# Kernel tuning notes

Measured on AMD Instinct MI355X. Metric: run time of the kernel, lower is better.

Reference implementation:

```python
import jax, jax.numpy as jnp
import numpy as np

N_EMBD = 2048
N_HEAD = 16
HEAD_DIM = N_EMBD // N_HEAD
BATCH = 2
SEQ = 2048


def setup_inputs() -> dict:
    key = jax.random.key(0)
    k1, k2, k3 = jax.random.split(key, 3)
    scale = 0.02
    return {
        "hidden_states": jax.random.normal(k1, (BATCH, SEQ, N_EMBD), dtype=jnp.float32),
        "c_attn_w": jax.random.normal(k2, (N_EMBD, 3 * N_EMBD), dtype=jnp.float32) * scale,
        "c_attn_b": jnp.zeros((3 * N_EMBD,), dtype=jnp.float32),
        "c_proj_w": jax.random.normal(k3, (N_EMBD, N_EMBD), dtype=jnp.float32) * scale,
        "c_proj_b": jnp.zeros((N_EMBD,), dtype=jnp.float32),
    }


def reference(hidden_states, c_attn_w, c_attn_b, c_proj_w, c_proj_b):
    B, S, E = hidden_states.shape
    # Fused QKV projection (Conv1D: x @ W + b)
    qkv = hidden_states @ c_attn_w + c_attn_b  # [B, S, 3E]
    q, k, v = jnp.split(qkv, 3, axis=-1)
    # split heads -> [B, H, S, D]
    def split_heads(t):
        return t.reshape(B, S, N_HEAD, HEAD_DIM).transpose(0, 2, 1, 3)
    q, k, v = split_heads(q), split_heads(k), split_heads(v)
    # scaled scores, causal mask, softmax (dropout p=0 -> identity)
    scores = jnp.einsum("bhqd,bhkd->bhqk", q, k) / jnp.asarray(
        HEAD_DIM ** 0.5, dtype=q.dtype)
    causal = jnp.tril(jnp.ones((S, S), dtype=bool))  # [S, S]
    mask_value = jnp.finfo(scores.dtype).min
    scores = jnp.where(causal[None, None, :, :], scores, mask_value)
    attn = jax.nn.softmax(scores, axis=-1)
    out = jnp.einsum("bhqk,bhkd->bhqd", attn, v)  # [B, H, S, D]
    # merge heads -> [B, S, E]
    out = out.transpose(0, 2, 1, 3).reshape(B, S, E)
    # output projection
    return out @ c_proj_w + c_proj_b
```

## Files before the change

kernel.cpp:

```cpp
#include <hip/hip_runtime.h>
#include <hip/hip_bf16.h>

typedef __bf16 bf16x8 __attribute__((ext_vector_type(8)));
typedef float f32x4 __attribute__((ext_vector_type(4)));

__device__ __forceinline__ float bf2f(unsigned short u) {
  union { unsigned int i; float f; } v; v.i = ((unsigned int)u) << 16; return v.f;
}
__device__ __forceinline__ unsigned short f2bf(float f) {
  union { unsigned int i; float f; } v; v.f = f;
  unsigned int i = v.i;
  return (unsigned short)((i + 0x7FFFu + ((i >> 16) & 1u)) >> 16);
}

typedef const __attribute__((address_space(1))) unsigned int* gas_ptr;
typedef __attribute__((address_space(3))) unsigned int* las_ptr;
__device__ __forceinline__ void gload_lds16(const unsigned short* g, unsigned short* l) {
  __builtin_amdgcn_global_load_lds((gas_ptr)(const void*)g, (las_ptr)(void*)l, 16, 0, 0);
}

__global__ __launch_bounds__(256) void detect_k(const unsigned short* __restrict__ h,
                                                int* __restrict__ flag) {
  __shared__ int s[256];
  int cnt = 0;
  for (int i = threadIdx.x; i < 4096; i += 256) {
    unsigned short u = h[2 * i];
    int e = (u >> 7) & 0xFF;
    if ((e >= 96 && e <= 140) || u == 0) cnt++;
  }
  s[threadIdx.x] = cnt;
  __syncthreads();
  for (int o = 128; o > 0; o >>= 1) {
    if (threadIdx.x < o) s[threadIdx.x] += s[threadIdx.x + o];
    __syncthreads();
  }
  if (threadIdx.x == 0) *flag = (s[0] >= 3600) ? 1 : 0;
}

__global__ __launch_bounds__(256) void cvt_hidden_k(const void* __restrict__ src,
                                                    unsigned short* __restrict__ dst, int n,
                                                    const int* __restrict__ flag) {
  if (*flag) return;
  for (int i = blockIdx.x * 256 + threadIdx.x; i < n; i += gridDim.x * 256)
    dst[i] = f2bf(((const float*)src)[i]);
}

__global__ __launch_bounds__(256) void transpose_w2_k(const void* __restrict__ w_qkv,
                                                      const void* __restrict__ w_proj,
                                                      unsigned short* __restrict__ dst_qkv,
                                                      unsigned short* __restrict__ dst_proj,
                                                      const int* __restrict__ flag) {
  __shared__ unsigned short tile[32][33];
  const int f = *flag;
  int bid = blockIdx.x;
  const void* src;
  unsigned short* dst;
  int R = 2048, C, cx, cy;
  if (bid < 12288) {
    src = w_qkv; dst = dst_qkv; C = 6144; cx = bid % 192; cy = bid / 192;
  } else {
    bid -= 12288;
    src = w_proj; dst = dst_proj; C = 2048; cx = bid % 64; cy = bid / 64;
  }
  const int x = threadIdx.x & 31;
  const int y = threadIdx.x >> 5;
  const int r0 = cy * 32, c0 = cx * 32;
#pragma unroll
  for (int i = 0; i < 4; i++) {
    size_t idx = (size_t)(r0 + y + 8 * i) * C + c0 + x;
    tile[y + 8 * i][x] = f ? ((const unsigned short*)src)[idx]
                           : f2bf(((const float*)src)[idx]);
  }
  __syncthreads();
#pragma unroll
  for (int i = 0; i < 4; i++)
    dst[(size_t)(c0 + y + 8 * i) * R + r0 + x] = tile[x][y + 8 * i];
}

__global__ __launch_bounds__(256) void transpose_v_k(const unsigned short* __restrict__ qkv,
                                                     unsigned short* __restrict__ Vt) {
  __shared__ unsigned short tile[32][33];
  const int bh = blockIdx.z;
  const int b = bh >> 4, hh = bh & 15;
  const int s0 = blockIdx.x * 32, d0 = blockIdx.y * 32;
  const int x = threadIdx.x & 31, y = threadIdx.x >> 5;
#pragma unroll
  for (int i = 0; i < 4; i++)
    tile[y + 8 * i][x] =
        qkv[((size_t)b * 2048 + s0 + y + 8 * i) * 6144 + 4096 + hh * 128 + d0 + x];
  __syncthreads();
#pragma unroll
  for (int i = 0; i < 4; i++)
    Vt[((size_t)bh * 128 + d0 + y + 8 * i) * 2048 + s0 + x] = tile[x][y + 8 * i];
}

__global__ __launch_bounds__(256) void gemm_bias_k(const unsigned short* __restrict__ A_bf,
                                                   const unsigned short* __restrict__ A_cvt,
                                                   const unsigned short* __restrict__ Bt,
                                                   const void* __restrict__ bias,
                                                   void* __restrict__ Cout,
                                                   int M, int N, int K,
                                                   const int* __restrict__ flag,
                                                   int final_out) {
  __shared__ __attribute__((aligned(16))) unsigned short As[128][64];
  __shared__ __attribute__((aligned(16))) unsigned short Bs[128][64];
  const int f = *flag;
  const unsigned short* A = f ? A_bf : A_cvt;
  const int t = threadIdx.x;
  const int wave = t >> 6, lane = t & 63;
  const int col = lane & 15, quad = lane >> 4;
  const int wm = wave >> 1, wn = wave & 1;
  const int m0 = blockIdx.y * 128, n0 = blockIdx.x * 128;
  const int srow = lane >> 3;
  const int schunk = ((lane & 7) ^ srow) * 8;
  const int rsw = col & 7;

  const f32x4 fzero = {0.f, 0.f, 0.f, 0.f};
  f32x4 acc[4][4];
#pragma unroll
  for (int i = 0; i < 4; i++)
#pragma unroll
    for (int j = 0; j < 4; j++) acc[i][j] = fzero;

  for (int k0 = 0; k0 < K; k0 += 64) {
    __syncthreads();
#pragma unroll
    for (int c = 0; c < 4; c++) {
      int seg = wave * 4 + c;
      int row = seg * 8 + srow;
      gload_lds16(&A [(size_t)(m0 + row) * K + k0 + schunk], &As[seg * 8][0]);
      gload_lds16(&Bt[(size_t)(n0 + row) * K + k0 + schunk], &Bs[seg * 8][0]);
    }
    __syncthreads();
#pragma unroll
    for (int ks = 0; ks < 2; ks++) {
      bf16x8 af[4], bfr[4];
#pragma unroll
      for (int i = 0; i < 4; i++)
        af[i] = *(const bf16x8*)&As[wm * 64 + i * 16 + col][(((ks << 2) | quad) ^ rsw) * 8];
#pragma unroll
      for (int j = 0; j < 4; j++)
        bfr[j] = *(const bf16x8*)&Bs[wn * 64 + j * 16 + col][(((ks << 2) | quad) ^ rsw) * 8];
#pragma unroll
      for (int i = 0; i < 4; i++)
#pragma unroll
        for (int j = 0; j < 4; j++)
          acc[i][j] = __builtin_amdgcn_mfma_f32_16x16x32_bf16(af[i], bfr[j], acc[i][j], 0, 0, 0);
    }
  }
  const int f32o = final_out ? (f == 0) : 0;
#pragma unroll
  for (int j = 0; j < 4; j++) {
    int n = n0 + wn * 64 + j * 16 + col;
    float bv = f ? bf2f(((const unsigned short*)bias)[n]) : ((const float*)bias)[n];
#pragma unroll
    for (int i = 0; i < 4; i++)
#pragma unroll
      for (int r = 0; r < 4; r++) {
        int m = m0 + wm * 64 + i * 16 + quad * 4 + r;
        float v = acc[i][j][r] + bv;
        if (f32o) ((float*)Cout)[(size_t)m * N + n] = v;
        else      ((unsigned short*)Cout)[(size_t)m * N + n] = f2bf(v);
      }
  }
}

#define ATT_SCALE 0.08838834764831845f
__global__ __launch_bounds__(256) void attn_k(const unsigned short* __restrict__ qkv,
                                              const unsigned short* __restrict__ Vt,
                                              unsigned short* __restrict__ O) {
  __shared__ __attribute__((aligned(16))) unsigned short Ks[64][136];
  __shared__ __attribute__((aligned(16))) unsigned short Vs[128][72];
  __shared__ __attribute__((aligned(16))) unsigned short Ps[4][16][72];
  const int t = threadIdx.x;
  const int wave = t >> 6, lane = t & 63;
  const int col = lane & 15, quad = lane >> 4;
  const int h = blockIdx.y, b = blockIdx.z;
  const size_t base = (size_t)b * 2048 * 6144;
  const size_t vbase = ((size_t)(b * 16 + h)) * 128 * 2048;
  const int hcol = h * 128;

  const int kr = t >> 2;
  const int kc = (t & 3) * 8;
  const int vr = t >> 1;
  const int vc = (t & 1) * 32;

  const f32x4 fzero = {0.f, 0.f, 0.f, 0.f};

  for (int pass = 0; pass < 2; pass++) {
    const int qt = pass ? (int)blockIdx.x : 31 - (int)blockIdx.x;

    bf16x8 qf[4];
    {
      size_t qrow = base + (size_t)(qt * 64 + wave * 16 + col) * 6144 + hcol;
#pragma unroll
      for (int ks = 0; ks < 4; ks++)
        qf[ks] = *(const bf16x8*)&qkv[qrow + ks * 32 + quad * 8];
    }

    f32x4 o[8];
#pragma unroll
    for (int i = 0; i < 8; i++) o[i] = fzero;
    float l_i[4] = {0.f, 0.f, 0.f, 0.f};

    __syncthreads();
    {
      size_t grow = base + (size_t)kr * 6144 + 2048 + hcol;
#pragma unroll
      for (int p = 0; p < 4; p++)
        *(bf16x8*)&Ks[kr][kc + p * 32] = *(const bf16x8*)&qkv[grow + kc + p * 32];
      size_t vrow = vbase + (size_t)vr * 2048;
#pragma unroll
      for (int c = 0; c < 4; c++)
        *(bf16x8*)&Vs[vr][vc + c * 8] = *(const bf16x8*)&Vt[vrow + vc + c * 8];
    }
    __syncthreads();

    for (int kt = 0; kt <= qt; kt++) {
      bf16x8 kreg[4], vreg[4];
      const bool pf = (kt < qt);
      if (pf) {
        size_t grow = base + (size_t)((kt + 1) * 64 + kr) * 6144 + 2048 + hcol;
#pragma unroll
        for (int p = 0; p < 4; p++)
          kreg[p] = *(const bf16x8*)&qkv[grow + kc + p * 32];
        size_t vrow = vbase + (size_t)vr * 2048 + (kt + 1) * 64;
#pragma unroll
        for (int c = 0; c < 4; c++)
          vreg[c] = *(const bf16x8*)&Vt[vrow + vc + c * 8];
      }

      f32x4 sc[4];
#pragma unroll
      for (int nb = 0; nb < 4; nb++) {
        f32x4 s = fzero;
#pragma unroll
        for (int ks = 0; ks < 4; ks++) {
          bf16x8 kf = *(const bf16x8*)&Ks[nb * 16 + col][ks * 32 + quad * 8];
          s = __builtin_amdgcn_mfma_f32_16x16x32_bf16(qf[ks], kf, s, 0, 0, 0);
        }
        sc[nb] = s;
      }

      const bool diag = (kt == qt);
#pragma unroll
      for (int nb = 0; nb < 4; nb++) {
        int kl = nb * 16 + col;
#pragma unroll
        for (int r = 0; r < 4; r++) {
          float s = sc[nb][r];
          if (diag && kl > wave * 16 + quad * 4 + r) s = -1e30f;
          float p = __expf(s * ATT_SCALE);
          l_i[r] += p;
          Ps[wave][quad * 4 + r][nb * 16 + col] = f2bf(p);
        }
      }
      bf16x8 pfr[2];
#pragma unroll
      for (int ks2 = 0; ks2 < 2; ks2++)
        pfr[ks2] = *(const bf16x8*)&Ps[wave][col][ks2 * 32 + quad * 8];
#pragma unroll
      for (int nbo = 0; nbo < 8; nbo++)
#pragma unroll
        for (int ks2 = 0; ks2 < 2; ks2++) {
          bf16x8 vf = *(const bf16x8*)&Vs[nbo * 16 + col][ks2 * 32 + quad * 8];
          o[nbo] = __builtin_amdgcn_mfma_f32_16x16x32_bf16(pfr[ks2], vf, o[nbo], 0, 0, 0);
        }

      __syncthreads();
      if (pf) {
#pragma unroll
        for (int p = 0; p < 4; p++)
          *(bf16x8*)&Ks[kr][kc + p * 32] = kreg[p];
#pragma unroll
        for (int c = 0; c < 4; c++)
          *(bf16x8*)&Vs[vr][vc + c * 8] = vreg[c];
      }
      __syncthreads();
    }

#pragma unroll
    for (int r = 0; r < 4; r++) {
#pragma unroll
      for (int off = 1; off < 16; off <<= 1)
        l_i[r] += __shfl_xor(l_i[r], off, 64);
      l_i[r] = 1.0f / l_i[r];
    }

#pragma unroll
    for (int nbo = 0; nbo < 8; nbo++)
#pragma unroll
      for (int r = 0; r < 4; r++) {
        int m = qt * 64 + wave * 16 + quad * 4 + r;
        O[((size_t)b * 2048 + m) * 2048 + hcol + nbo * 16 + col] = f2bf(o[nbo][r] * l_i[r]);
      }
  }
}

extern "C" void kernel_launch(void* const* d_in, const int* in_sizes, int n_in,
                              void* d_out, int out_size, void* d_ws, size_t ws_size,
                              hipStream_t stream) {
  (void)in_sizes; (void)n_in; (void)out_size; (void)ws_size;
  int* flag = (int*)d_ws;
  unsigned short* wsu = (unsigned short*)d_ws + 128;
  unsigned short* Wt_qkv    = wsu;
  unsigned short* Wt_proj   = Wt_qkv + (size_t)6144 * 2048;
  unsigned short* QKV       = Wt_proj + (size_t)2048 * 2048;
  unsigned short* hidden_bf = QKV + (size_t)4096 * 6144;
  unsigned short* Obuf      = Wt_qkv;
  unsigned short* Vt        = hidden_bf + (size_t)4096 * 2048;

  detect_k<<<1, 256, 0, stream>>>((const unsigned short*)d_in[0], flag);
  cvt_hidden_k<<<2048, 256, 0, stream>>>(d_in[0], hidden_bf, 4096 * 2048, flag);
  transpose_w2_k<<<16384, 256, 0, stream>>>(d_in[1], d_in[3], Wt_qkv, Wt_proj, flag);
  gemm_bias_k<<<dim3(48, 32), 256, 0, stream>>>((const unsigned short*)d_in[0], hidden_bf,
                                                Wt_qkv, d_in[2], QKV,
                                                4096, 6144, 2048, flag, 0);
  transpose_v_k<<<dim3(64, 4, 32), 256, 0, stream>>>(QKV, Vt);
  attn_k<<<dim3(16, 16, 2), 256, 0, stream>>>(QKV, Vt, Obuf);
  gemm_bias_k<<<dim3(16, 32), 256, 0, stream>>>(Obuf, Obuf, Wt_proj, d_in[4], d_out,
                                                4096, 2048, 2048, flag, 1);
}
```

Baseline: 415.9 us.

## Add 256x256-tile double-buffered MFMA GEMM kernel for the QKV projection

Adds a new GEMM kernel with 256x256 output tiles computed by 512 threads (8 waves). It double-buffers LDS via direct global-to-LDS loads, uses an XOR-swizzled shared layout, and remaps workgroup IDs into 8 chunks for better L2 locality. Loads for the next k-tile are interleaved with MFMA phases, and s_setprio raises priority during the MFMA phases. The QKV projection uses this kernel in place of the 128x128 version, aiming for higher arithmetic intensity and better latency hiding. The cost is more LDS (128KB) and more accumulator registers, which limits occupancy, and the grid is 384 blocks.

Result: no change. 423.6 us (+1.9%).

```diff
diff --git a/kernel.cpp b/kernel.cpp
--- a/kernel.cpp
+++ b/kernel.cpp
@@ -92,6 +92,163 @@
 #pragma unroll
   for (int i = 0; i < 4; i++)
     Vt[((size_t)bh * 128 + d0 + y + 8 * i) * 2048 + s0 + x] = tile[x][y + 8 * i];
+}
+
+__global__ __launch_bounds__(512, 2) void gemm256_k(const unsigned short* __restrict__ A_bf,
+                                                    const unsigned short* __restrict__ A_cvt,
+                                                    const unsigned short* __restrict__ Bt,
+                                                    const void* __restrict__ bias,
+                                                    unsigned short* __restrict__ Cout,
+                                                    int M, int N, int K,
+                                                    const int* __restrict__ flag) {
+  __shared__ __attribute__((aligned(16))) unsigned short As[2][2][128][64];
+  __shared__ __attribute__((aligned(16))) unsigned short Bs[2][2][128][64];
+  const int f = *flag;
+  const unsigned short* Ap = f ? A_bf : A_cvt;
+  const int t = threadIdx.x;
+  const int wave = t >> 6, lane = t & 63;
+  const int col = lane & 15, quad = lane >> 4;
+  const int wm = wave >> 2, wn = wave & 3;
+
+  const int nbx = N >> 8;
+  int wgid = blockIdx.y * nbx + blockIdx.x;
+  const int nwg = (M >> 8) * nbx;
+  if ((nwg & 7) == 0) {
+    const int cpx = nwg >> 3;
+    wgid = (wgid & 7) * cpx + (wgid >> 3);
+  }
+  const int n0 = (wgid % nbx) << 8;
+  const int m0 = (wgid / nbx) << 8;
+
+  const int srow = lane >> 3;
+  const int sx = ((lane & 7) ^ srow) * 8;
+  const int rsw = col & 7;
+
+  const unsigned short* pA = Ap + (size_t)(m0 + wave * 16 + srow) * K + sx;
+  const unsigned short* pB = Bt + (size_t)(n0 + wave * 16 + srow) * K + sx;
+  const int NT = K >> 6;
+
+#define STAGE_A(d, h, kt)                                                                  \
+  do {                                                                                     \
+    gload_lds16(pA + (size_t)((h) * 128) * K + (kt) * 64, &As[(d)][(h)][wave * 16][0]);    \
+    gload_lds16(pA + (size_t)((h) * 128 + 8) * K + (kt) * 64,                              \
+                &As[(d)][(h)][wave * 16 + 8][0]);                                          \
+  } while (0)
+#define STAGE_B(d, h, kt)                                                                  \
+  do {                                                                                     \
+    gload_lds16(pB + (size_t)((h) * 128) * K + (kt) * 64, &Bs[(d)][(h)][wave * 16][0]);    \
+    gload_lds16(pB + (size_t)((h) * 128 + 8) * K + (kt) * 64,                              \
+                &Bs[(d)][(h)][wave * 16 + 8][0]);                                          \
+  } while (0)
+#define LDA(d, rf, kk) \
+  (*(const bf16x8*)&As[(d)][wm][(rf) * 16 + col][((((kk) << 2) | quad) ^ rsw) * 8])
+#define LDB(d, cf, kk) \
+  (*(const bf16x8*)&Bs[(d)][wn >> 1][(wn & 1) * 64 + (cf) * 16 + col][((((kk) << 2) | quad) ^ rsw) * 8])
+
+  const f32x4 fzero = {0.f, 0.f, 0.f, 0.f};
+  f32x4 acc[8][4];
+#pragma unroll
+  for (int i = 0; i < 8; i++)
+#pragma unroll
+    for (int j = 0; j < 4; j++) acc[i][j] = fzero;
+
+  STAGE_A(0, 0, 0); STAGE_A(0, 1, 0);
+  STAGE_B(0, 0, 0); STAGE_B(0, 1, 0);
+  STAGE_A(1, 0, 1); STAGE_A(1, 1, 1);
+  asm volatile("s_waitcnt vmcnt(4)" ::: "memory");
+  __builtin_amdgcn_sched_barrier(0);
+  __builtin_amdgcn_s_barrier();
+
+  for (int u = 0; u < NT; ++u) {
+    const int d = u & 1;
+    bf16x8 a0[4][2], a1[4][2], b0[2][2], b1[2][2];
+
+#pragma unroll
+    for (int rf = 0; rf < 4; rf++) { a0[rf][0] = LDA(d, rf, 0); a0[rf][1] = LDA(d, rf, 1); }
+#pragma unroll
+    for (int cf = 0; cf < 2; cf++) { b0[cf][0] = LDB(d, cf, 0); b0[cf][1] = LDB(d, cf, 1); }
+    if (u + 1 < NT) STAGE_B(d ^ 1, 0, u + 1);
+    __builtin_amdgcn_s_barrier();
+    asm volatile("s_waitcnt lgkmcnt(0)" ::: "memory");
+    __builtin_amdgcn_sched_barrier(0);
+    __builtin_amdgcn_s_setprio(1);
+#pragma unroll
+    for (int rf = 0; rf < 4; rf++)
+#pragma unroll
+      for (int cf = 0; cf < 2; cf++) {
+        acc[rf][cf] = __builtin_amdgcn_mfma_f32_16x16x32_bf16(a0[rf][0], b0[cf][0], acc[rf][cf], 0, 0, 0);
+        acc[rf][cf] = __builtin_amdgcn_mfma_f32_16x16x32_bf16(a0[rf][1], b0[cf][1], acc[rf][cf], 0, 0, 0);
+      }
+    __builtin_amdgcn_s_setprio(0);
+    __builtin_amdgcn_s_barrier();
+
+#pragma unroll
+    for (int rf = 0; rf < 4; rf++) { a1[rf][0] = LDA(d, rf + 4, 0); a1[rf][1] = LDA(d, rf + 4, 1); }
+    if (u + 1 < NT) STAGE_B(d ^ 1, 1, u + 1);
+    __builtin_amdgcn_s_barrier();
+    asm volatile("s_waitcnt lgkmcnt(0)" ::: "memory");
+    __builtin_amdgcn_sched_barrier(0);
+    __builtin_amdgcn_s_setprio(1);
+#pragma unroll
+    for (int rf = 0; rf < 4; rf++)
+#pragma unroll
+      for (int cf = 0; cf < 2; cf++) {
+        acc[rf + 4][cf] = __builtin_amdgcn_mfma_f32_16x16x32_bf16(a1[rf][0], b0[cf][0], acc[rf + 4][cf], 0, 0, 0);
+        acc[rf + 4][cf] = __builtin_amdgcn_mfma_f32_16x16x32_bf16(a1[rf][1], b0[cf][1], acc[rf + 4][cf], 0, 0, 0);
+      }
+    __builtin_amdgcn_s_setprio(0);
+    __builtin_amdgcn_s_barrier();
+
+#pragma unroll
+    for (int cf = 0; cf < 2; cf++) { b1[cf][0] = LDB(d, cf + 2, 0); b1[cf][1] = LDB(d, cf + 2, 1); }
+    if (u + 2 < NT) STAGE_A(d, 0, u + 2);
+    __builtin_amdgcn_s_barrier();
+    asm volatile("s_waitcnt lgkmcnt(0)" ::: "memory");
+    __builtin_amdgcn_sched_barrier(0);
+    __builtin_amdgcn_s_setprio(1);
+#pragma unroll
+    for (int rf = 0; rf < 4; rf++)
+#pragma unroll
+      for (int cf = 0; cf < 2; cf++) {
+        acc[rf][cf + 2] = __builtin_amdgcn_mfma_f32_16x16x32_bf16(a0[rf][0], b1[cf][0], acc[rf][cf + 2], 0, 0, 0);
+        acc[rf][cf + 2] = __builtin_amdgcn_mfma_f32_16x16x32_bf16(a0[rf][1], b1[cf][1], acc[rf][cf + 2], 0, 0, 0);
+      }
+    __builtin_amdgcn_s_setprio(0);
+    __builtin_amdgcn_s_barrier();
+
+    if (u + 2 < NT) STAGE_A(d, 1, u + 2);
+    __builtin_amdgcn_s_setprio(1);
+#pragma unroll
+    for (int rf = 0; rf < 4; rf++)
+#pragma unroll
+      for (int cf = 0; cf < 2; cf++) {
+        acc[rf + 4][cf + 2] = __builtin_amdgcn_mfma_f32_16x16x32_bf16(a1[rf][0], b1[cf][0], acc[rf + 4][cf + 2], 0, 0, 0);
+        acc[rf + 4][cf + 2] = __builtin_amdgcn_mfma_f32_16x16x32_bf16(a1[rf][1], b1[cf][1], acc[rf + 4][cf + 2], 0, 0, 0);
+      }
+    __builtin_amdgcn_s_setprio(0);
+    if (u + 2 < NT) asm volatile("s_waitcnt vmcnt(4)" ::: "memory");
+    else            asm volatile("s_waitcnt vmcnt(0)" ::: "memory");
+    __builtin_amdgcn_sched_barrier(0);
+    __builtin_amdgcn_s_barrier();
+  }
+#undef STAGE_A
+#undef STAGE_B
+#undef LDA
+#undef LDB
+
+  const int nbase = n0 + wn * 64;
+#pragma unroll
+  for (int cf = 0; cf < 4; cf++) {
+    int n = nbase + cf * 16 + col;
+    float bv = f ? bf2f(((const unsigned short*)bias)[n]) : ((const float*)bias)[n];
+#pragma unroll
+    for (int rf = 0; rf < 8; rf++)
+#pragma unroll
+      for (int r = 0; r < 4; r++) {
+        int m = m0 + wm * 128 + rf * 16 + quad * 4 + r;
+        Cout[(size_t)m * N + n] = f2bf(acc[rf][cf][r] + bv);
+      }
+  }
 }
 
 __global__ __launch_bounds__(256) void gemm_bias_k(const unsigned short* __restrict__ A_bf,
@@ -313,9 +470,9 @@
   detect_k<<<1, 256, 0, stream>>>((const unsigned short*)d_in[0], flag);
   cvt_hidden_k<<<2048, 256, 0, stream>>>(d_in[0], hidden_bf, 4096 * 2048, flag);
   transpose_w2_k<<<16384, 256, 0, stream>>>(d_in[1], d_in[3], Wt_qkv, Wt_proj, flag);
-  gemm_bias_k<<<dim3(48, 32), 256, 0, stream>>>((const unsigned short*)d_in[0], hidden_bf,
-                                                Wt_qkv, d_in[2], QKV,
-                                                4096, 6144, 2048, flag, 0);
+  gemm256_k<<<dim3(24, 16), 512, 0, stream>>>((const unsigned short*)d_in[0], hidden_bf,
+                                              Wt_qkv, d_in[2], QKV,
+                                              4096, 6144, 2048, flag);
   transpose_v_k<<<dim3(64, 4, 32), 256, 0, stream>>>(QKV, Vt);
   attn_k<<<dim3(16, 16, 2), 256, 0, stream>>>(QKV, Vt, Obuf);
   gemm_bias_k<<<dim3(16, 32), 256, 0, stream>>>(Obuf, Obuf, Wt_proj, d_in[4], d_out,
```

## Add dedicated QKV GEMM kernel with 256x192 tiles and double-buffered async LDS pipeline

Applied to the files above, without the earlier changes.

Replaces the generic 128x128 GEMM for the QKV projection with a dedicated 512-thread kernel using 256x192 tiles. It double-buffers A and B in LDS through direct global-to-LDS loads with XOR swizzling, and interleaves staging with MFMA phases under explicit waitcnt, barriers and setprio. It also remaps workgroup IDs in an XCD-aware way to improve L2 locality. The aim is to hide memory latency and raise MFMA utilisation, at the cost of complex hand-tuned vmcnt/lgkmcnt counts that must stay exactly right, plus higher LDS and register use.

After: 389.1 us. 6.4% less time.

```diff
diff --git a/kernel.cpp b/kernel.cpp
--- a/kernel.cpp
+++ b/kernel.cpp
@@ -92,6 +92,166 @@
 #pragma unroll
   for (int i = 0; i < 4; i++)
     Vt[((size_t)bh * 128 + d0 + y + 8 * i) * 2048 + s0 + x] = tile[x][y + 8 * i];
+}
+
+__global__ __launch_bounds__(512, 2) void gemm_qkv_k(const unsigned short* __restrict__ A_bf,
+                                                     const unsigned short* __restrict__ A_cvt,
+                                                     const unsigned short* __restrict__ Bt,
+                                                     const void* __restrict__ bias,
+                                                     unsigned short* __restrict__ Cout,
+                                                     int M, int N, int K,
+                                                     const int* __restrict__ flag) {
+  __shared__ __attribute__((aligned(16))) unsigned short As[2][256][64];
+  __shared__ __attribute__((aligned(16))) unsigned short Bs[2][192][64];
+  const int f = *flag;
+  const unsigned short* Ap = f ? A_bf : A_cvt;
+  const int t = threadIdx.x;
+  const int wave = t >> 6, lane = t & 63;
+  const int col = lane & 15, quad = lane >> 4;
+  const int wm = wave >> 1, wn = wave & 1;
+
+  const int nbx = N / 192;
+  int wgid = blockIdx.y * nbx + blockIdx.x;
+  const int nwg = (M >> 8) * nbx;
+  if ((nwg & 7) == 0) {
+    const int cpx = nwg >> 3;
+    wgid = (wgid & 7) * cpx + (wgid >> 3);
+  }
+  const int n0 = (wgid % nbx) * 192;
+  const int m0 = (wgid / nbx) << 8;
+
+  const int srow = lane >> 3;
+  const int sx = ((lane & 7) ^ srow) * 8;
+  const int rsw = col & 7;
+
+  const unsigned short* pA = Ap + (size_t)(m0 + wave * 8 + srow) * K + sx;
+  const unsigned short* pB = Bt + (size_t)(n0 + wave * 8 + srow) * K + sx;
+  const int NT = K >> 6;
+
+#define STAGE_A(d, q, kt) \
+  gload_lds16(pA + (size_t)((q) * 64) * K + (size_t)(kt) * 64, &As[(d)][(q) * 64 + wave * 8][0])
+#define STAGE_B(d, q, kt) \
+  gload_lds16(pB + (size_t)((q) * 64) * K + (size_t)(kt) * 64, &Bs[(d)][(q) * 64 + wave * 8][0])
+#define LDA(d, rf, kk) \
+  (*(const bf16x8*)&As[(d)][wm * 64 + (rf) * 16 + col][((((kk) << 2) | quad) ^ rsw) * 8])
+#define LDB(d, cf, kk) \
+  (*(const bf16x8*)&Bs[(d)][wn * 96 + (cf) * 16 + col][((((kk) << 2) | quad) ^ rsw) * 8])
+
+  const f32x4 fzero = {0.f, 0.f, 0.f, 0.f};
+  f32x4 acc[4][6];
+#pragma unroll
+  for (int i = 0; i < 4; i++)
+#pragma unroll
+    for (int j = 0; j < 6; j++) acc[i][j] = fzero;
+
+  bf16x8 aA[4][2], aB[4][2];
+
+  STAGE_A(0, 0, 0); STAGE_A(0, 1, 0); STAGE_A(0, 2, 0); STAGE_A(0, 3, 0);
+  STAGE_B(0, 0, 0); STAGE_B(0, 1, 0); STAGE_B(0, 2, 0);
+  STAGE_A(1, 0, 1); STAGE_A(1, 1, 1); STAGE_A(1, 2, 1); STAGE_A(1, 3, 1);
+  asm volatile("s_waitcnt vmcnt(4)" ::: "memory");
+  __builtin_amdgcn_sched_barrier(0);
+  __builtin_amdgcn_s_barrier();
+
+#define BODY(D, U, FIRST, SB, SA, VM2, VM3, PRER, ACUR, ANXT)                              \
+  {                                                                                        \
+                                            \
+    if (FIRST) {                                                                           \
+      _Pragma("unroll") for (int rf = 0; rf < 4; rf++) {                                   \
+        ACUR[rf][0] = LDA(D, rf, 0);                                                       \
+        ACUR[rf][1] = LDA(D, rf, 1);                                                       \
+      }                                                                                    \
+    }                                                                                      \
+    bf16x8 b01[2][2];                                                                      \
+    _Pragma("unroll") for (int c = 0; c < 2; c++) {                                        \
+      b01[c][0] = LDB(D, c, 0);                                                            \
+      b01[c][1] = LDB(D, c, 1);                                                            \
+    }                                                                                      \
+    if (SB) { STAGE_B((D) ^ 1, 0, (U) + 1); STAGE_B((D) ^ 1, 1, (U) + 1); }                \
+    __builtin_amdgcn_s_barrier();                                                          \
+    asm volatile("s_waitcnt lgkmcnt(0)" ::: "memory");                                     \
+    __builtin_amdgcn_sched_barrier(0);                                                     \
+    __builtin_amdgcn_s_setprio(1);                                                         \
+    _Pragma("unroll") for (int rf = 0; rf < 4; rf++)                                       \
+      _Pragma("unroll") for (int c = 0; c < 2; c++) {                                      \
+        acc[rf][c] = __builtin_amdgcn_mfma_f32_16x16x32_bf16(ACUR[rf][0], b01[c][0], acc[rf][c], 0, 0, 0); \
+        acc[rf][c] = __builtin_amdgcn_mfma_f32_16x16x32_bf16(ACUR[rf][1], b01[c][1], acc[rf][c], 0, 0, 0); \
+      }                                                                                    \
+    __builtin_amdgcn_s_setprio(0);                                                         \
+                                            \
+    bf16x8 b23[2][2];                                                                      \
+    _Pragma("unroll") for (int c = 0; c < 2; c++) {                                        \
+      b23[c][0] = LDB(D, (c) + 2, 0);                                                      \
+      b23[c][1] = LDB(D, (c) + 2, 1);                                                      \
+    }                                                                                      \
+    if (SB) STAGE_B((D) ^ 1, 2, (U) + 1);                                                  \
+    if (SA) { STAGE_A(D, 0, (U) + 2); STAGE_A(D, 1, (U) + 2); }                            \
+    asm volatile("s_waitcnt " VM2 ::: "memory");                                           \
+    __builtin_amdgcn_s_barrier();                                                          \
+    asm volatile("s_waitcnt lgkmcnt(0)" ::: "memory");                                     \
+    __builtin_amdgcn_sched_barrier(0);                                                     \
+    __builtin_amdgcn_s_setprio(1);                                                         \
+    _Pragma("unroll") for (int rf = 0; rf < 4; rf++)                                       \
+      _Pragma("unroll") for (int c = 0; c < 2; c++) {                                      \
+        acc[rf][(c) + 2] = __builtin_amdgcn_mfma_f32_16x16x32_bf16(ACUR[rf][0], b23[c][0], acc[rf][(c) + 2], 0, 0, 0); \
+        acc[rf][(c) + 2] = __builtin_amdgcn_mfma_f32_16x16x32_bf16(ACUR[rf][1], b23[c][1], acc[rf][(c) + 2], 0, 0, 0); \
+      }                                                                                    \
+    __builtin_amdgcn_s_setprio(0);                                                         \
+                                            \
+    bf16x8 b45[2][2];                                                                      \
+    _Pragma("unroll") for (int c = 0; c < 2; c++) {                                        \
+      b45[c][0] = LDB(D, (c) + 4, 0);                                                      \
+      b45[c][1] = LDB(D, (c) + 4, 1);                                                      \
+    }                                                                                      \
+    __builtin_amdgcn_sched_barrier(0);  \
+    if (PRER) {                                                                            \
+      _Pragma("unroll") for (int rf = 0; rf < 4; rf++) {                                   \
+        ANXT[rf][0] = LDA((D) ^ 1, rf, 0);                                                 \
+        ANXT[rf][1] = LDA((D) ^ 1, rf, 1);                                                 \
+      }                                                                                    \
+    }                                                                                      \
+    if (SA) { STAGE_A(D, 2, (U) + 2); STAGE_A(D, 3, (U) + 2); }                            \
+    asm volatile("s_waitcnt " VM3 ::: "memory");                                           \
+    __builtin_amdgcn_s_barrier();                                                          \
+    if (PRER) asm volatile("s_waitcnt lgkmcnt(8)" ::: "memory");                           \
+    else      asm volatile("s_waitcnt lgkmcnt(0)" ::: "memory");                           \
+    __builtin_amdgcn_sched_barrier(0);                                                     \
+    __builtin_amdgcn_s_setprio(1);                                                         \
+    _Pragma("unroll") for (int rf = 0; rf < 4; rf++)                                       \
+      _Pragma("unroll") for (int c = 0; c < 2; c++) {                                      \
+        acc[rf][(c) + 4] = __builtin_amdgcn_mfma_f32_16x16x32_bf16(ACUR[rf][0], b45[c][0], acc[rf][(c) + 4], 0, 0, 0); \
+        acc[rf][(c) + 4] = __builtin_amdgcn_mfma_f32_16x16x32_bf16(ACUR[rf][1], b45[c][1], acc[rf][(c) + 4], 0, 0, 0); \
+      }                                                                                    \
+    __builtin_amdgcn_s_setprio(0);                                                         \
+  }
+
+  BODY(0, 0, 1, 1, 1, "vmcnt(5)", "vmcnt(4)", 1, aA, aB)
+  BODY(1, 1, 0, 1, 1, "vmcnt(5)", "vmcnt(4)", 1, aB, aA)
+  for (int u2 = 2; u2 + 3 < NT; u2 += 2) {
+    BODY(0, u2, 0, 1, 1, "vmcnt(5)", "vmcnt(4)", 1, aA, aB)
+    BODY(1, u2 + 1, 0, 1, 1, "vmcnt(5)", "vmcnt(4)", 1, aB, aA)
+  }
+  BODY(0, NT - 2, 0, 1, 0, "vmcnt(3)", "vmcnt(0)", 1, aA, aB)
+  BODY(1, NT - 1, 0, 0, 0, "vmcnt(0)", "vmcnt(0)", 0, aB, aA)
+
+#undef BODY
+#undef STAGE_A
+#undef STAGE_B
+#undef LDA
+#undef LDB
+
+#pragma unroll
+  for (int cf = 0; cf < 6; cf++) {
+    int n = n0 + wn * 96 + cf * 16 + col;
+    float bv = f ? bf2f(((const unsigned short*)bias)[n]) : ((const float*)bias)[n];
+#pragma unroll
+    for (int rf = 0; rf < 4; rf++)
+#pragma unroll
+      for (int r = 0; r < 4; r++) {
+        int m = m0 + wm * 64 + rf * 16 + quad * 4 + r;
+        Cout[(size_t)m * N + n] = f2bf(acc[rf][cf][r] + bv);
+      }
+  }
 }
 
 __global__ __launch_bounds__(256) void gemm_bias_k(const unsigned short* __restrict__ A_bf,
@@ -313,9 +473,9 @@
   detect_k<<<1, 256, 0, stream>>>((const unsigned short*)d_in[0], flag);
   cvt_hidden_k<<<2048, 256, 0, stream>>>(d_in[0], hidden_bf, 4096 * 2048, flag);
   transpose_w2_k<<<16384, 256, 0, stream>>>(d_in[1], d_in[3], Wt_qkv, Wt_proj, flag);
-  gemm_bias_k<<<dim3(48, 32), 256, 0, stream>>>((const unsigned short*)d_in[0], hidden_bf,
-                                                Wt_qkv, d_in[2], QKV,
-                                                4096, 6144, 2048, flag, 0);
+  gemm_qkv_k<<<dim3(32, 16), 512, 0, stream>>>((const unsigned short*)d_in[0], hidden_bf,
+                                               Wt_qkv, d_in[2], QKV,
+                                               4096, 6144, 2048, flag);
   transpose_v_k<<<dim3(64, 4, 32), 256, 0, stream>>>(QKV, Vt);
   attn_k<<<dim3(16, 16, 2), 256, 0, stream>>>(QKV, Vt, Obuf);
   gemm_bias_k<<<dim3(16, 32), 256, 0, stream>>>(Obuf, Obuf, Wt_proj, d_in[4], d_out,
```
